# Performance work log

Measured on AMD Instinct MI355X. Metric: run time of the kernel, lower is better.

The kernel has to match this reference:

```python
import jax, jax.numpy as jnp
import numpy as np

B, H, S, D = 4, 16, 1024, 64
MAX_REL = 128
VOCAB = 2 * MAX_REL + 1  # relative-position vocabulary


def setup_inputs() -> dict:
    key = jax.random.key(0)
    k1, k2, k3, k4 = jax.random.split(key, 4)
    tensor = jax.random.normal(k1, (B, H, S, D), dtype=jnp.float32)
    rel_keys_emb = jax.random.normal(k2, (VOCAB, D), dtype=jnp.float32) * 0.02
    rel_values_emb = jax.random.normal(k3, (VOCAB, D), dtype=jnp.float32) * 0.02
    # nn.Parameter initialized xavier_uniform_ on shape (1, H, 1, 1)
    bias = jax.random.uniform(k4, (1, H, 1, 1), dtype=jnp.float32, minval=-1.0, maxval=1.0)
    return {
        "tensor": tensor,
        "rel_keys_emb": rel_keys_emb,
        "rel_values_emb": rel_values_emb,
        "bias": bias,
        "max_relative_position": MAX_REL,
    }


def reference(tensor, rel_keys_emb, rel_values_emb, bias, max_relative_position):
    # forward(tensor, is_key=True, transpose=False)
    seq_len = tensor.shape[2]
    r = jnp.arange(seq_len)
    dist = jnp.clip(r[None, :] - r[:, None], -max_relative_position, max_relative_position)
    idx = dist + max_relative_position          # [S, S] in [0, 2*max_rel]
    rel_emb = rel_keys_emb[idx]                 # [S, S, D] gathered table
    # original: [S, B*H, D] @ [S, D, S] -> [S, B*H, S] -> [B, H, S, S]
    scores = jnp.einsum('bhsd,std->bhst', tensor, rel_emb)
    return scores + bias
```

## Files before the change

### kernel.cpp

```cpp
#include <hip/hip_runtime.h>
#include <hip/hip_bf16.h>


constexpr int S_   = 1024;
constexpr int D_   = 64;
constexpr int VOC  = 257;
constexpr int BQ   = 64;
constexpr int CSTR = 66;

typedef __attribute__((ext_vector_type(8))) short short8;
typedef __attribute__((ext_vector_type(4))) float f32x4;

__device__ __forceinline__ unsigned short f2bf(float x) {
  unsigned u = __float_as_uint(x);
  return (unsigned short)((u + 0x7fffu + ((u >> 16) & 1u)) >> 16);
}

__device__ __forceinline__ short8 pack8(float4 a, float4 b) {
  short8 r;
  r[0] = (short)f2bf(a.x); r[1] = (short)f2bf(a.y);
  r[2] = (short)f2bf(a.z); r[3] = (short)f2bf(a.w);
  r[4] = (short)f2bf(b.x); r[5] = (short)f2bf(b.y);
  r[6] = (short)f2bf(b.z); r[7] = (short)f2bf(b.w);
  return r;
}

__device__ __forceinline__ unsigned packpair(float lo, float hi) {
  return (unsigned)f2bf(lo) | ((unsigned)f2bf(hi) << 16);
}

__global__ __launch_bounds__(256, 4)
void relpos_mfma(const float* __restrict__ tensor,
                 const float* __restrict__ relk,
                 const float* __restrict__ bias,
                 float* __restrict__ out) {
  __shared__ __align__(16) unsigned short c_lds[VOC * CSTR + 6];

  const int tid  = threadIdx.x;
  const int lane = tid & 63;
  const int w    = tid >> 6;
  const int bh   = blockIdx.x >> 4;
  const int s0   = (blockIdx.x & 15) * BQ;
  const int h    = bh & 15;
  const int l15  = lane & 15;
  const int l4   = lane >> 4;

  const float* xrow = tensor + ((size_t)(bh * S_ + s0 + 16 * w + l15)) * D_ + l4 * 8;
  short8 a0, a1;
  {
    float4 p0 = *reinterpret_cast<const float4*>(xrow);
    float4 p1 = *reinterpret_cast<const float4*>(xrow + 4);
    a0 = pack8(p0, p1);
    float4 q0 = *reinterpret_cast<const float4*>(xrow + 32);
    float4 q1 = *reinterpret_cast<const float4*>(xrow + 36);
    a1 = pack8(q0, q1);
  }

  const float bv = bias[h];

#pragma unroll 4
  for (int nt = 0; nt < 17; ++nt) {
    const int vrow = 16 * nt + l15;
    const int erow = vrow > 256 ? 256 : vrow;
    const float* ep = relk + (size_t)erow * D_ + l4 * 8;
    float4 e00 = *reinterpret_cast<const float4*>(ep);
    float4 e01 = *reinterpret_cast<const float4*>(ep + 4);
    float4 e10 = *reinterpret_cast<const float4*>(ep + 32);
    float4 e11 = *reinterpret_cast<const float4*>(ep + 36);
    short8 b0 = pack8(e00, e01);
    short8 b1 = pack8(e10, e11);

    f32x4 acc = {0.f, 0.f, 0.f, 0.f};
    acc = __builtin_amdgcn_mfma_f32_16x16x32_bf16(a0, b0, acc, 0, 0, 0);
    acc = __builtin_amdgcn_mfma_f32_16x16x32_bf16(a1, b1, acc, 0, 0, 0);

    if (vrow <= 256) {
      const int row0 = 16 * w + l4 * 4;
      unsigned* cp = reinterpret_cast<unsigned*>(&c_lds[vrow * CSTR + row0]);
      cp[0] = packpair(acc[0] + bv, acc[1] + bv);
      cp[1] = packpair(acc[2] + bv, acc[3] + bv);
    }
  }
  __syncthreads();

  float* orow = out + ((size_t)bh * S_ + (size_t)s0) * S_;
  int vb = 128 - s0;
  for (int rr = 0; rr < BQ; ++rr) {
#pragma unroll
    for (int j = 0; j < 4; ++j) {
      const int t = tid + 256 * j;
      int v = t + vb;
      v = v < 0 ? 0 : (v > 256 ? 256 : v);
      orow[t] = __uint_as_float(((unsigned)c_lds[v * CSTR + rr]) << 16);
    }
    orow += S_;
    --vb;
  }
}

extern "C" void kernel_launch(void* const* d_in, const int* in_sizes, int n_in,
                              void* d_out, int out_size, void* d_ws, size_t ws_size,
                              hipStream_t stream) {
  const float* tensor = (const float*)d_in[0];
  const float* relk   = (const float*)d_in[1];
  const float* bias   = (const float*)d_in[3];
  float* out          = (float*)d_out;

  const int B = 4, H = 16;
  dim3 grid(B * H * (S_ / BQ));
  dim3 block(256);
  relpos_mfma<<<grid, block, 0, stream>>>(tensor, relk, bias, out);
}
```

Before: 73.40 us.

## Store per-wave skewed LDS rows and write output with vectorized float4 band/constant regions

Each wave now writes its MFMA results into its own LDS region, row-major and skewed by row index, so later reads are aligned uint2 loads. This removes the block-wide __syncthreads. The output phase has each wave emit its 16 rows with float4 stores. Regions outside the relative-position band are filled with broadcast constants, and only the band is read from LDS, which replaces the per-element clamped gather and scalar stores. The cost is more complex index arithmetic, scalar fixups at unaligned band edges, and per-wave divergence in the stores.

New measurement: 79.41 us. +8.2%, slower.

```diff
diff --git a/kernel.cpp b/kernel.cpp
--- a/kernel.cpp
+++ b/kernel.cpp
@@ -1,12 +1,10 @@
 #include <hip/hip_runtime.h>
-#include <hip/hip_bf16.h>
 
 
 constexpr int S_   = 1024;
 constexpr int D_   = 64;
-constexpr int VOC  = 257;
 constexpr int BQ   = 64;
-constexpr int CSTR = 66;
+constexpr int CPAD = 264;
 
 typedef __attribute__((ext_vector_type(8))) short short8;
 typedef __attribute__((ext_vector_type(4))) float f32x4;
@@ -15,7 +13,9 @@
   unsigned u = __float_as_uint(x);
   return (unsigned short)((u + 0x7fffu + ((u >> 16) & 1u)) >> 16);
 }
-
+__device__ __forceinline__ float bfu2f(unsigned short h) {
+  return __uint_as_float(((unsigned)h) << 16);
+}
 __device__ __forceinline__ short8 pack8(float4 a, float4 b) {
   short8 r;
   r[0] = (short)f2bf(a.x); r[1] = (short)f2bf(a.y);
@@ -25,16 +25,12 @@
   return r;
 }
 
-__device__ __forceinline__ unsigned packpair(float lo, float hi) {
-  return (unsigned)f2bf(lo) | ((unsigned)f2bf(hi) << 16);
-}
-
 __global__ __launch_bounds__(256, 4)
-void relpos_mfma(const float* __restrict__ tensor,
-                 const float* __restrict__ relk,
-                 const float* __restrict__ bias,
-                 float* __restrict__ out) {
-  __shared__ __align__(16) unsigned short c_lds[VOC * CSTR + 6];
+void relpos_v3(const float* __restrict__ tensor,
+               const float* __restrict__ relk,
+               const float* __restrict__ bias,
+               float* __restrict__ out) {
+  __shared__ __align__(16) unsigned short c_lds[4 * 16 * CPAD];
 
   const int tid  = threadIdx.x;
   const int lane = tid & 63;
@@ -45,56 +41,92 @@
   const int l15  = lane & 15;
   const int l4   = lane >> 4;
 
+  unsigned short* cw = c_lds + w * 16 * CPAD;
+
   const float* xrow = tensor + ((size_t)(bh * S_ + s0 + 16 * w + l15)) * D_ + l4 * 8;
-  short8 a0, a1;
-  {
-    float4 p0 = *reinterpret_cast<const float4*>(xrow);
-    float4 p1 = *reinterpret_cast<const float4*>(xrow + 4);
-    a0 = pack8(p0, p1);
-    float4 q0 = *reinterpret_cast<const float4*>(xrow + 32);
-    float4 q1 = *reinterpret_cast<const float4*>(xrow + 36);
-    a1 = pack8(q0, q1);
-  }
-
+  short8 a0 = pack8(*reinterpret_cast<const float4*>(xrow),
+                    *reinterpret_cast<const float4*>(xrow + 4));
+  short8 a1 = pack8(*reinterpret_cast<const float4*>(xrow + 32),
+                    *reinterpret_cast<const float4*>(xrow + 36));
   const float bv = bias[h];
 
-#pragma unroll 4
   for (int nt = 0; nt < 17; ++nt) {
-    const int vrow = 16 * nt + l15;
-    const int erow = vrow > 256 ? 256 : vrow;
+    const int vcol = 16 * nt + l15;
+    const int erow = vcol > 256 ? 256 : vcol;
     const float* ep = relk + (size_t)erow * D_ + l4 * 8;
-    float4 e00 = *reinterpret_cast<const float4*>(ep);
-    float4 e01 = *reinterpret_cast<const float4*>(ep + 4);
-    float4 e10 = *reinterpret_cast<const float4*>(ep + 32);
-    float4 e11 = *reinterpret_cast<const float4*>(ep + 36);
-    short8 b0 = pack8(e00, e01);
-    short8 b1 = pack8(e10, e11);
-
+    short8 b0 = pack8(*reinterpret_cast<const float4*>(ep),
+                      *reinterpret_cast<const float4*>(ep + 4));
+    short8 b1 = pack8(*reinterpret_cast<const float4*>(ep + 32),
+                      *reinterpret_cast<const float4*>(ep + 36));
     f32x4 acc = {0.f, 0.f, 0.f, 0.f};
     acc = __builtin_amdgcn_mfma_f32_16x16x32_bf16(a0, b0, acc, 0, 0, 0);
     acc = __builtin_amdgcn_mfma_f32_16x16x32_bf16(a1, b1, acc, 0, 0, 0);
-
-    if (vrow <= 256) {
-      const int row0 = 16 * w + l4 * 4;
-      unsigned* cp = reinterpret_cast<unsigned*>(&c_lds[vrow * CSTR + row0]);
-      cp[0] = packpair(acc[0] + bv, acc[1] + bv);
-      cp[1] = packpair(acc[2] + bv, acc[3] + bv);
+    if (vcol <= 256) {
+      const int r0 = l4 * 4;
+#pragma unroll
+      for (int i = 0; i < 4; ++i) {
+        cw[(r0 + i) * CPAD + i + vcol] = f2bf(acc[i] + bv);
+      }
     }
   }
-  __syncthreads();
 
-  float* orow = out + ((size_t)bh * S_ + (size_t)s0) * S_;
-  int vb = 128 - s0;
-  for (int rr = 0; rr < BQ; ++rr) {
-#pragma unroll
-    for (int j = 0; j < 4; ++j) {
-      const int t = tid + 256 * j;
-      int v = t + vb;
-      v = v < 0 ? 0 : (v > 256 ? 256 : v);
-      orow[t] = __uint_as_float(((unsigned)c_lds[v * CSTR + rr]) << 16);
+#pragma unroll 4
+  for (int rl = 0; rl < 16; ++rl) {
+    const int s   = s0 + 16 * w + rl;
+    const int pad = rl & 3;
+    const unsigned short* cr = cw + rl * CPAD;
+    float* orow = out + ((size_t)bh * S_ + s) * (size_t)S_;
+
+    const float c0f   = bfu2f(cr[pad]);
+    const float c256f = bfu2f(cr[pad + 256]);
+    const float4 c0v   = make_float4(c0f, c0f, c0f, c0f);
+    const float4 c256v = make_float4(c256f, c256f, c256f, c256f);
+
+    const int w0  = s - 128 < 0 ? 0 : s - 128;
+    const int w1  = s + 129 > S_ ? S_ : s + 129;
+    const int La  = w0 & ~3;
+    const int w0a = (w0 + 3) & ~3;
+    const int w1a = w1 & ~3;
+    const int Ra  = (w1 + 3) & ~3;
+
+    const int nL = La >> 2;
+    for (int j = 0; 64 * j < nL; ++j) {
+      int slot = lane + 64 * j;
+      if (slot < nL)
+        *reinterpret_cast<float4*>(&orow[4 * slot]) = c0v;
     }
-    orow += S_;
-    --vb;
+    const int nR = (S_ - Ra) >> 2;
+    for (int j = 0; 64 * j < nR; ++j) {
+      int slot = lane + 64 * j;
+      if (slot < nR)
+        *reinterpret_cast<float4*>(&orow[Ra + 4 * slot]) = c256v;
+    }
+    const int n4 = (w1a - w0a) >> 2;
+    for (int j = 0; j < 2; ++j) {
+      int slot = lane + 64 * j;
+      if (slot < n4) {
+        int t0 = w0a + 4 * slot;
+        int vI = t0 - s + 128 + pad;
+        uint2 q = *reinterpret_cast<const uint2*>(&cr[vI]);
+        float4 o;
+        o.x = __uint_as_float(q.x << 16);
+        o.y = __uint_as_float(q.x & 0xffff0000u);
+        o.z = __uint_as_float(q.y << 16);
+        o.w = __uint_as_float(q.y & 0xffff0000u);
+        *reinterpret_cast<float4*>(&orow[t0]) = o;
+      }
+    }
+    if (lane < 8) {
+      const bool left  = (w0 & 3) != 0;
+      const bool right = (w1 & 3) != 0;
+      const bool act   = (lane < 4) ? left : right;
+      if (act) {
+        int t = (lane < 4) ? (La + lane) : (w1a + (lane - 4));
+        int v = t - s + 128;
+        v = v < 0 ? 0 : (v > 256 ? 256 : v);
+        orow[t] = bfu2f(cr[pad + v]);
+      }
+    }
   }
 }
 
@@ -109,5 +141,5 @@
   const int B = 4, H = 16;
   dim3 grid(B * H * (S_ / BQ));
   dim3 block(256);
-  relpos_mfma<<<grid, block, 0, stream>>>(tensor, relk, bias, out);
+  relpos_v3<<<grid, block, 0, stream>>>(tensor, relk, bias, out);
 }
```
